# Kernel tuning notes

Measured on AMD Instinct MI355X. Metric: run time of the kernel, lower is better.

## Reference

```python
import jax, jax.numpy as jnp
import numpy as np

NUM_GROUPS = 8
EPS = 1e-6


def group_norm(x, gamma, beta):
    # x: [B, C, N] flattened spatial; GroupNorm over (channels-in-group, spatial)
    B, C, N = x.shape
    xg = x.reshape(B, NUM_GROUPS, C // NUM_GROUPS, N)
    mean = xg.mean(axis=(2, 3), keepdims=True)
    var = xg.var(axis=(2, 3), keepdims=True)
    xn = ((xg - mean) * jax.lax.rsqrt(var + EPS)).reshape(B, C, N)
    return xn * gamma[None, :, None] + beta[None, :, None]


def setup_inputs() -> dict:
    key = jax.random.key(0)
    ks = jax.random.split(key, 3)
    B, C, H, W, D = 4, 128, 16, 16, 16
    x = jax.random.normal(ks[0], (B, C, H, W, D), dtype=jnp.float32)
    gamma = jnp.ones((C,), dtype=jnp.float32)
    beta = jnp.zeros((C,), dtype=jnp.float32)
    init_scale = 0.1
    # default_init(scale): variance-scaling ~ scale/fan_avg uniform; approximate with scaled normal
    w_qkv = jax.random.normal(ks[1], (3 * C, C), dtype=jnp.float32) * np.sqrt(init_scale / C)
    b_qkv = jnp.zeros((3 * C,), dtype=jnp.float32)
    w_proj = jax.random.normal(ks[2], (C, C), dtype=jnp.float32) * np.sqrt(init_scale / C)
    b_proj = jnp.zeros((C,), dtype=jnp.float32)
    return {"x": x, "gamma": gamma, "beta": beta, "w_qkv": w_qkv,
            "b_qkv": b_qkv, "w_proj": w_proj, "b_proj": b_proj}


def reference(x, gamma, beta, w_qkv, b_qkv, w_proj, b_proj):
    B, C, H, W, D = x.shape
    N = H * W * D
    xf = x.reshape(B, C, N)
    xn = group_norm(xf, gamma, beta)
    # 1x1 Conv3d == channel GEMM: [3C, C] @ [B, C, N]
    qkv = jnp.einsum('oc,bcn->bon', w_qkv, xn) + b_qkv[None, :, None]
    q, k, v = jnp.split(qkv, 3, axis=1)  # each [B, C, N]
    scale = float(C) ** (-0.5)
    w = jnp.einsum('bcq,bck->bqk', q, k) * scale  # [B, N, N]
    w = jax.nn.softmax(w, axis=-1)
    h = jnp.einsum('bqk,bck->bcq', w, v)  # [B, C, N]
    h = jnp.einsum('oc,bcn->bon', w_proj, h) + b_proj[None, :, None]
    out = xf + h  # skip_scale = 1.0 (skip_scale=False)
    return out.reshape(B, C, H, W, D)
```

## Files before the change

### kernel.cpp

```cpp
#include <hip/hip_runtime.h>

typedef __bf16 bf16_t;
typedef bf16_t bf16x8 __attribute__((ext_vector_type(8)));
typedef float f32x4 __attribute__((ext_vector_type(4)));
typedef float f32x16 __attribute__((ext_vector_type(16)));
typedef unsigned short u16;
typedef unsigned int u32;

__device__ __forceinline__ float bfu2f(u32 h) {
  union { u32 u; float f; } v; v.u = h << 16;
  return v.f;
}
__device__ __forceinline__ void gll16(const void* g, void* l) {
  __builtin_amdgcn_global_load_lds((const __attribute__((address_space(1))) unsigned int*)g,
                                   (__attribute__((address_space(3))) unsigned int*)l, 16, 0, 0);
}
__device__ __forceinline__ u32 cvtpk(float lo, float hi) {
  u32 r;
  asm("v_cvt_pk_bf16_f32 %0, %1, %2" : "=v"(r) : "v"(lo), "v"(hi));
  return r;
}

__global__ __launch_bounds__(256) void gn_stats(const float* __restrict__ x,
                                                float* __restrict__ partial) {
  int bg = blockIdx.x >> 4, ck = blockIdx.x & 15;
  int tid = threadIdx.x;
  const float4* base = reinterpret_cast<const float4*>(x + (size_t)bg * 65536 + ck * 4096);
  float s = 0.f, sq = 0.f;
  #pragma unroll
  for (int j = 0; j < 4; ++j) {
    float4 v = base[j * 256 + tid];
    s += v.x + v.y + v.z + v.w;
    sq += v.x * v.x + v.y * v.y + v.z * v.z + v.w * v.w;
  }
  #pragma unroll
  for (int off = 32; off > 0; off >>= 1) {
    s += __shfl_down(s, off);
    sq += __shfl_down(sq, off);
  }
  __shared__ float red[8];
  int wid = tid >> 6;
  if ((tid & 63) == 0) { red[wid] = s; red[4 + wid] = sq; }
  __syncthreads();
  if (tid == 0) {
    float ts = red[0] + red[1] + red[2] + red[3];
    float tq = red[4] + red[5] + red[6] + red[7];
    partial[(bg * 16 + ck) * 2] = ts;
    partial[(bg * 16 + ck) * 2 + 1] = tq;
  }
}

__global__ __launch_bounds__(256) void gn_norm(const float* __restrict__ x,
                                               const float* __restrict__ gamma,
                                               const float* __restrict__ beta,
                                               const float* __restrict__ partial,
                                               u16* __restrict__ xnt) {
  int b = blockIdx.x >> 6, nc = blockIdx.x & 63;
  int tid = threadIdx.x;
  int cbase = (tid & 15) * 8;
  int g = cbase >> 4;
  float s = 0.f, sq = 0.f;
  #pragma unroll
  for (int k = 0; k < 16; ++k) {
    s += partial[((b * 8 + g) * 16 + k) * 2];
    sq += partial[((b * 8 + g) * 16 + k) * 2 + 1];
  }
  float mean = s * (1.f / 65536.f);
  float var = sq * (1.f / 65536.f) - mean * mean;
  float rstd = rsqrtf(var + 1e-6f);
  float ga[8], be[8];
  #pragma unroll
  for (int j = 0; j < 8; ++j) {
    ga[j] = gamma[cbase + j] * rstd;
    be[j] = beta[cbase + j] - mean * ga[j];
  }
  int n0 = nc * 64;
  #pragma unroll
  for (int it = 0; it < 4; ++it) {
    int n = n0 + it * 16 + (tid >> 4);
    union { u16 s[8]; uint4 u; } pk;
    #pragma unroll
    for (int j = 0; j < 8; ++j) {
      float v = x[((size_t)(b * 128 + cbase + j)) * 4096 + n] * ga[j] + be[j];
      pk.s[j] = __builtin_bit_cast(u16, (bf16_t)v);
    }
    *reinterpret_cast<uint4*>(xnt + ((size_t)(b * 4096 + n)) * 128 + cbase) = pk.u;
  }
}

__global__ __launch_bounds__(256) void qkv_kernel(const float* __restrict__ wq,
                                                  const float* __restrict__ bq,
                                                  const u16* __restrict__ xnt,
                                                  u16* __restrict__ qt,
                                                  u16* __restrict__ kt,
                                                  u16* __restrict__ vv) {
  __shared__ char aS[16384];
  __shared__ char bS[16384];
  int b = blockIdx.z;
  int o0 = blockIdx.y * 64;
  int n0 = blockIdx.x * 64;
  int tid = threadIdx.x;
  #pragma unroll
  for (int i = 0; i < 8; ++i) {
    int chunk = tid + (i << 8);
    int o = chunk >> 5, cj = (chunk & 31) << 2;
    float4 f = *reinterpret_cast<const float4*>(wq + (o0 + o) * 128 + cj);
    u16 h0 = __builtin_bit_cast(u16, (bf16_t)f.x);
    u16 h1 = __builtin_bit_cast(u16, (bf16_t)f.y);
    u16 h2 = __builtin_bit_cast(u16, (bf16_t)f.z);
    u16 h3 = __builtin_bit_cast(u16, (bf16_t)f.w);
    *reinterpret_cast<ushort4*>(aS + ((o * 256 + cj * 2) ^ ((o & 7) << 4))) = make_ushort4(h0, h1, h2, h3);
  }
  #pragma unroll
  for (int i = 0; i < 4; ++i) {
    int chunk = tid + (i << 8);
    int n = chunk >> 4, ch = chunk & 15;
    uint4 d = *reinterpret_cast<const uint4*>(xnt + ((size_t)(b * 4096 + n0 + n)) * 128 + ch * 8);
    *reinterpret_cast<uint4*>(bS + ((n * 256 + ch * 16) ^ ((n & 7) << 4))) = d;
  }
  __syncthreads();
  int w = tid >> 6, l = tid & 63, lr = l & 15, lg = l >> 4;
  f32x4 acc[4] = {{0,0,0,0},{0,0,0,0},{0,0,0,0},{0,0,0,0}};
  int orow = 16 * w + lr;
  #pragma unroll
  for (int kc = 0; kc < 4; ++kc) {
    int c2 = (lg * 8 + 32 * kc) * 2;
    bf16x8 a = *reinterpret_cast<const bf16x8*>(aS + ((orow * 256 + c2) ^ ((orow & 7) << 4)));
    #pragma unroll
    for (int fn = 0; fn < 4; ++fn) {
      int n = lr + 16 * fn;
      bf16x8 bb = *reinterpret_cast<const bf16x8*>(bS + ((n * 256 + c2) ^ ((n & 7) << 4)));
      acc[fn] = __builtin_amdgcn_mfma_f32_16x16x32_bf16(a, bb, acc[fn], 0, 0, 0);
    }
  }
  const float alpha = 0.12753325f;
  if (o0 < 256) {
    bool isq = (o0 < 128);
    __syncthreads();
    u16* tS = (u16*)aS;
    #pragma unroll
    for (int fn = 0; fn < 4; ++fn) {
      #pragma unroll
      for (int j = 0; j < 4; ++j) {
        int o_loc = 16 * w + lg * 4 + j;
        int n_loc = lr + 16 * fn;
        float v = acc[fn][j] + bq[o0 + o_loc];
        if (isq) v *= alpha;
        tS[o_loc * 68 + n_loc] = __builtin_bit_cast(u16, (bf16_t)v);
      }
    }
    __syncthreads();
    u16* dst = isq ? qt : kt;
    int obase = o0 & 127;
    #pragma unroll
    for (int it = 0; it < 2; ++it) {
      int n_l = (tid >> 3) + it * 32;
      int oc = (tid & 7) * 8;
      union { u16 s[8]; uint4 u; } pk;
      #pragma unroll
      for (int k2 = 0; k2 < 8; ++k2) pk.s[k2] = tS[(oc + k2) * 68 + n_l];
      *reinterpret_cast<uint4*>(dst + ((size_t)(b * 4096 + n0 + n_l)) * 128 + obase + oc) = pk.u;
    }
  } else {
    #pragma unroll
    for (int fn = 0; fn < 4; ++fn) {
      #pragma unroll
      for (int j = 0; j < 4; ++j) {
        int o_loc = 16 * w + lg * 4 + j;
        int n = n0 + lr + 16 * fn;
        float v = acc[fn][j] + bq[o0 + o_loc];
        ((bf16_t*)vv)[((size_t)(b * 128 + (o0 - 256) + o_loc)) * 4096 + n] = (bf16_t)v;
      }
    }
  }
}

__global__ __launch_bounds__(256, 2) void attn_kernel(const u16* __restrict__ qt,
                                                      const u16* __restrict__ kt,
                                                      const u16* __restrict__ vv,
                                                      u16* __restrict__ opart,
                                                      float* __restrict__ ml) {
  __shared__ char kS[2][16384];
  __shared__ char vS[2][16384];
  int b = blockIdx.z;
  int sp = blockIdx.y;
  int q0 = blockIdx.x * 128;
  int tid = threadIdx.x;
  int w = tid >> 6, l = tid & 63, lq = l & 31, h = l >> 5;

  bf16x8 qf[8];
  {
    const u16* qrow = qt + ((size_t)(b * 4096 + q0 + w * 32 + lq)) * 128 + h * 8;
    #pragma unroll
    for (int cs = 0; cs < 8; ++cs)
      qf[cs] = *reinterpret_cast<const bf16x8*>(qrow + cs * 16);
  }
  f32x16 acc[4];
  #pragma unroll
  for (int cc = 0; cc < 4; ++cc)
    #pragma unroll
    for (int i = 0; i < 16; ++i) acc[cc][i] = 0.f;
  float m2 = -1e30f, lsum = 0.f;

  const u16* ktb = kt + ((size_t)(b * 4096 + sp * 1024)) * 128;
  const u16* vvb = vv + ((size_t)b * 128) * 4096 + sp * 1024;

  auto stage = [&](int bufi, int kti) {
    #pragma unroll
    for (int i = 0; i < 4; ++i) {
      int n = (tid >> 4) + i * 16;
      int ck = (tid & 15) ^ (n & 7);
      gll16(ktb + (size_t)(kti * 64 + n) * 128 + ck * 8, kS[bufi] + tid * 16 + i * 4096);
    }
    #pragma unroll
    for (int i = 0; i < 4; ++i) {
      int c = (tid >> 3) + i * 32;
      int ck = (tid & 7) ^ (c & 7);
      gll16(vvb + (size_t)c * 4096 + kti * 64 + ck * 8, vS[bufi] + tid * 16 + i * 4096);
    }
  };

  stage(0, 0);
  __syncthreads();
  int buf = 0;

  for (int kti = 0; kti < 16; ++kti) {
    if (kti < 15) stage(buf ^ 1, kti + 1);

    f32x16 st0, st1;
    #pragma unroll
    for (int i = 0; i < 16; ++i) { st0[i] = 0.f; st1[i] = 0.f; }
    __builtin_amdgcn_s_setprio(1);
    #pragma unroll
    for (int cs = 0; cs < 8; ++cs) {
      int co = cs * 32 + h * 16;
      bf16x8 kf0 = *reinterpret_cast<const bf16x8*>(kS[buf] + ((lq * 256 + co) ^ ((lq & 7) << 4)));
      st0 = __builtin_amdgcn_mfma_f32_32x32x16_bf16(kf0, qf[cs], st0, 0, 0, 0);
      int kr1 = 32 + lq;
      bf16x8 kf1 = *reinterpret_cast<const bf16x8*>(kS[buf] + ((kr1 * 256 + co) ^ ((kr1 & 7) << 4)));
      st1 = __builtin_amdgcn_mfma_f32_32x32x16_bf16(kf1, qf[cs], st1, 0, 0, 0);
    }
    __builtin_amdgcn_s_setprio(0);

    float mt = st0[0];
    #pragma unroll
    for (int i = 1; i < 16; ++i) mt = fmaxf(mt, st0[i]);
    #pragma unroll
    for (int i = 0; i < 16; ++i) mt = fmaxf(mt, st1[i]);
    mt = fmaxf(mt, __shfl_xor(mt, 32));
    if (__any(mt > m2 + 8.f)) {
      float mn = fmaxf(m2, mt);
      float r = exp2f(m2 - mn);
      m2 = mn;
      lsum *= r;
      #pragma unroll
      for (int reg = 0; reg < 16; ++reg) {
        int qrow = (reg & 3) + 8 * (reg >> 2) + 4 * h;
        float rq = __shfl(r, qrow);
        #pragma unroll
        for (int cc = 0; cc < 4; ++cc) acc[cc][reg] *= rq;
      }
    }
    bf16x8 pa[4];
    #pragma unroll
    for (int ks = 0; ks < 2; ++ks) {
      float p[16];
      #pragma unroll
      for (int i = 0; i < 16; ++i) {
        float sv = (ks == 0) ? st0[i] : st1[i];
        p[i] = exp2f(sv - m2);
        lsum += p[i];
      }
      #pragma unroll
      for (int kk = 0; kk < 2; ++kk) {
        int r0 = kk * 8, r1 = kk * 8 + 4;
        u32 a1 = cvtpk(p[r0 + 0], p[r0 + 1]);
        u32 a2 = cvtpk(p[r0 + 2], p[r0 + 3]);
        u32 b1 = cvtpk(p[r1 + 0], p[r1 + 1]);
        u32 b2 = cvtpk(p[r1 + 2], p[r1 + 3]);
        u32 sa1 = (u32)__shfl_xor((int)a1, 32);
        u32 sa2 = (u32)__shfl_xor((int)a2, 32);
        u32 sb1 = (u32)__shfl_xor((int)b1, 32);
        u32 sb2 = (u32)__shfl_xor((int)b2, 32);
        union { u32 wd[4]; bf16x8 v; } af;
        af.wd[0] = h ? sb1 : a1;
        af.wd[1] = h ? sb2 : a2;
        af.wd[2] = h ? b1 : sa1;
        af.wd[3] = h ? b2 : sa2;
        pa[ks * 2 + kk] = af.v;
      }
    }
    __builtin_amdgcn_s_setprio(1);
    #pragma unroll
    for (int ks2 = 0; ks2 < 4; ++ks2) {
      int ko = ks2 * 32 + h * 16;
      #pragma unroll
      for (int cc = 0; cc < 4; ++cc) {
        int c = cc * 32 + lq;
        bf16x8 vf = *reinterpret_cast<const bf16x8*>(vS[buf] + ((c * 128 + ko) ^ ((c & 7) << 4)));
        acc[cc] = __builtin_amdgcn_mfma_f32_32x32x16_bf16(pa[ks2], vf, acc[cc], 0, 0, 0);
      }
    }
    __builtin_amdgcn_s_setprio(0);
    __syncthreads();
    buf ^= 1;
  }
  lsum += __shfl_xor(lsum, 32);
  #pragma unroll
  for (int reg = 0; reg < 16; ++reg) {
    int qrow = (reg & 3) + 8 * (reg >> 2) + 4 * h;
    size_t row = (size_t)(sp * 16384 + b * 4096 + q0 + w * 32 + qrow);
    bf16_t* orow = (bf16_t*)opart + row * 128 + lq;
    #pragma unroll
    for (int cc = 0; cc < 4; ++cc)
      orow[cc * 32] = (bf16_t)acc[cc][reg];
  }
  if (l < 32) {
    size_t row = (size_t)(sp * 16384 + b * 4096 + q0 + w * 32 + l);
    ml[row * 2] = m2;
    ml[row * 2 + 1] = lsum;
  }
}

__global__ __launch_bounds__(256) void proj_kernel(const float* __restrict__ wp,
                                                   const float* __restrict__ bp,
                                                   const u16* __restrict__ opart,
                                                   const float* __restrict__ ml,
                                                   const float* __restrict__ x,
                                                   float* __restrict__ out) {
  __shared__ char aS[16384];
  __shared__ char bS[16384];
  int b = blockIdx.z;
  int o0 = blockIdx.y * 64;
  int n0 = blockIdx.x * 64;
  int tid = threadIdx.x;
  #pragma unroll
  for (int i = 0; i < 8; ++i) {
    int chunk = tid + (i << 8);
    int o = chunk >> 5, cj = (chunk & 31) << 2;
    float4 f = *reinterpret_cast<const float4*>(wp + (o0 + o) * 128 + cj);
    u16 h0 = __builtin_bit_cast(u16, (bf16_t)f.x);
    u16 h1 = __builtin_bit_cast(u16, (bf16_t)f.y);
    u16 h2 = __builtin_bit_cast(u16, (bf16_t)f.z);
    u16 h3 = __builtin_bit_cast(u16, (bf16_t)f.w);
    *reinterpret_cast<ushort4*>(aS + ((o * 256 + cj * 2) ^ ((o & 7) << 4))) = make_ushort4(h0, h1, h2, h3);
  }
  #pragma unroll
  for (int i = 0; i < 4; ++i) {
    int chunk = tid + (i << 8);
    int n = chunk >> 4, ch = chunk & 15;
    size_t bn = (size_t)(b * 4096 + n0 + n);
    float m[4], lv[4];
    #pragma unroll
    for (int s = 0; s < 4; ++s) {
      m[s] = ml[((size_t)(s * 16384) + bn) * 2];
      lv[s] = ml[((size_t)(s * 16384) + bn) * 2 + 1];
    }
    float M = fmaxf(fmaxf(m[0], m[1]), fmaxf(m[2], m[3]));
    float wgt[4], L = 0.f;
    #pragma unroll
    for (int s = 0; s < 4; ++s) {
      wgt[s] = exp2f(m[s] - M);
      L += wgt[s] * lv[s];
    }
    float inv = 1.f / L;
    float o[8] = {0.f, 0.f, 0.f, 0.f, 0.f, 0.f, 0.f, 0.f};
    #pragma unroll
    for (int s = 0; s < 4; ++s) {
      uint4 pr = *reinterpret_cast<const uint4*>(opart + ((size_t)(s * 16384) + bn) * 128 + ch * 8);
      o[0] += wgt[s] * bfu2f(pr.x & 0xffffu);
      o[1] += wgt[s] * bfu2f(pr.x >> 16);
      o[2] += wgt[s] * bfu2f(pr.y & 0xffffu);
      o[3] += wgt[s] * bfu2f(pr.y >> 16);
      o[4] += wgt[s] * bfu2f(pr.z & 0xffffu);
      o[5] += wgt[s] * bfu2f(pr.z >> 16);
      o[6] += wgt[s] * bfu2f(pr.w & 0xffffu);
      o[7] += wgt[s] * bfu2f(pr.w >> 16);
    }
    u16 hh[8];
    #pragma unroll
    for (int e = 0; e < 8; ++e) hh[e] = __builtin_bit_cast(u16, (bf16_t)(o[e] * inv));
    uint4 packed;
    packed.x = (u32)hh[0] | ((u32)hh[1] << 16);
    packed.y = (u32)hh[2] | ((u32)hh[3] << 16);
    packed.z = (u32)hh[4] | ((u32)hh[5] << 16);
    packed.w = (u32)hh[6] | ((u32)hh[7] << 16);
    *reinterpret_cast<uint4*>(bS + ((n * 256 + ch * 16) ^ ((n & 7) << 4))) = packed;
  }
  __syncthreads();
  int w = tid >> 6, l = tid & 63, lr = l & 15, lg = l >> 4;
  f32x4 acc[4] = {{0,0,0,0},{0,0,0,0},{0,0,0,0},{0,0,0,0}};
  int orow = 16 * w + lr;
  #pragma unroll
  for (int kc = 0; kc < 4; ++kc) {
    int c2 = (lg * 8 + 32 * kc) * 2;
    bf16x8 a = *reinterpret_cast<const bf16x8*>(aS + ((orow * 256 + c2) ^ ((orow & 7) << 4)));
    #pragma unroll
    for (int fn = 0; fn < 4; ++fn) {
      int n = lr + 16 * fn;
      bf16x8 bb = *reinterpret_cast<const bf16x8*>(bS + ((n * 256 + c2) ^ ((n & 7) << 4)));
      acc[fn] = __builtin_amdgcn_mfma_f32_16x16x32_bf16(a, bb, acc[fn], 0, 0, 0);
    }
  }
  #pragma unroll
  for (int fn = 0; fn < 4; ++fn) {
    #pragma unroll
    for (int j = 0; j < 4; ++j) {
      int o = o0 + 16 * w + lg * 4 + j;
      int n = n0 + lr + 16 * fn;
      size_t idx = ((size_t)(b * 128 + o)) * 4096 + n;
      out[idx] = acc[fn][j] + bp[o] + x[idx];
    }
  }
}

extern "C" void kernel_launch(void* const* d_in, const int* in_sizes, int n_in,
                              void* d_out, int out_size, void* d_ws, size_t ws_size,
                              hipStream_t stream) {
  const float* x      = (const float*)d_in[0];
  const float* gamma  = (const float*)d_in[1];
  const float* beta   = (const float*)d_in[2];
  const float* w_qkv  = (const float*)d_in[3];
  const float* b_qkv  = (const float*)d_in[4];
  const float* w_proj = (const float*)d_in[5];
  const float* b_proj = (const float*)d_in[6];
  float* out = (float*)d_out;

  char* ws = (char*)d_ws;
  u16* xnt   = (u16*)(ws);
  u16* qt    = (u16*)(ws + (4u << 20));
  u16* kt    = (u16*)(ws + (8u << 20));
  u16* vv    = (u16*)(ws + (12u << 20));
  u16* opart = (u16*)(ws + (16u << 20));
  float* ml    = (float*)(ws + (48u << 20));
  float* parts = (float*)(ws + (49u << 20));

  hipLaunchKernelGGL(gn_stats, dim3(512), dim3(256), 0, stream, x, parts);
  hipLaunchKernelGGL(gn_norm, dim3(256), dim3(256), 0, stream, x, gamma, beta, parts, xnt);
  hipLaunchKernelGGL(qkv_kernel, dim3(64, 6, 4), dim3(256), 0, stream, w_qkv, b_qkv, xnt, qt, kt, vv);
  hipLaunchKernelGGL(attn_kernel, dim3(32, 4, 4), dim3(256), 0, stream, qt, kt, vv, opart, ml);
  hipLaunchKernelGGL(proj_kernel, dim3(64, 2, 4), dim3(256), 0, stream, w_proj, b_proj, opart, ml, x, out);
}
```

Baseline: 142.4 us.

## Coalesce GroupNorm transpose via LDS and reuse xnt tile across QKV outputs

gn_norm now reads x rows with contiguous float4 loads per channel. It transposes through a padded shared-memory tile, then writes xnt rows with 16-byte vector stores, replacing the strided scalar global reads. qkv_kernel now loops over three 64-row output chunks per block, so the xnt tile is staged once per block instead of once per chunk, and the grid shrinks from 6 to 2 in y. The cost is fewer blocks (512 instead of 1536), which means less parallelism, plus extra barriers per loop iteration and a separate shared transpose buffer.

```diff
diff --git a/kernel.cpp b/kernel.cpp
--- a/kernel.cpp
+++ b/kernel.cpp
@@ -55,10 +55,13 @@
                                                const float* __restrict__ beta,
                                                const float* __restrict__ partial,
                                                u16* __restrict__ xnt) {
+  __shared__ alignas(16) u16 tS[64 * 136];
   int b = blockIdx.x >> 6, nc = blockIdx.x & 63;
+  int n0 = nc * 64;
   int tid = threadIdx.x;
-  int cbase = (tid & 15) * 8;
-  int g = cbase >> 4;
+  int c = tid >> 1;
+  int nh = (tid & 1) * 32;
+  int g = c >> 4;
   float s = 0.f, sq = 0.f;
   #pragma unroll
   for (int k = 0; k < 16; ++k) {
@@ -68,24 +71,24 @@
   float mean = s * (1.f / 65536.f);
   float var = sq * (1.f / 65536.f) - mean * mean;
   float rstd = rsqrtf(var + 1e-6f);
-  float ga[8], be[8];
-  #pragma unroll
-  for (int j = 0; j < 8; ++j) {
-    ga[j] = gamma[cbase + j] * rstd;
-    be[j] = beta[cbase + j] - mean * ga[j];
-  }
-  int n0 = nc * 64;
-  #pragma unroll
-  for (int it = 0; it < 4; ++it) {
-    int n = n0 + it * 16 + (tid >> 4);
-    union { u16 s[8]; uint4 u; } pk;
-    #pragma unroll
-    for (int j = 0; j < 8; ++j) {
-      float v = x[((size_t)(b * 128 + cbase + j)) * 4096 + n] * ga[j] + be[j];
-      pk.s[j] = __builtin_bit_cast(u16, (bf16_t)v);
-    }
-    *reinterpret_cast<uint4*>(xnt + ((size_t)(b * 4096 + n)) * 128 + cbase) = pk.u;
-  }
+  float ga = gamma[c] * rstd;
+  float be = beta[c] - mean * ga;
+  const float4* xr4 = reinterpret_cast<const float4*>(x + ((size_t)(b * 128 + c)) * 4096 + n0 + nh);
+  #pragma unroll
+  for (int i = 0; i < 8; ++i) {
+    float4 v = xr4[i];
+    int nb = nh + i * 4;
+    tS[(nb + 0) * 136 + c] = __builtin_bit_cast(u16, (bf16_t)(v.x * ga + be));
+    tS[(nb + 1) * 136 + c] = __builtin_bit_cast(u16, (bf16_t)(v.y * ga + be));
+    tS[(nb + 2) * 136 + c] = __builtin_bit_cast(u16, (bf16_t)(v.z * ga + be));
+    tS[(nb + 3) * 136 + c] = __builtin_bit_cast(u16, (bf16_t)(v.w * ga + be));
+  }
+  __syncthreads();
+  int n = tid >> 2, cq = (tid & 3) * 32;
+  const uint4* src = reinterpret_cast<const uint4*>(tS + n * 136 + cq);
+  uint4 a0 = src[0], a1 = src[1], a2 = src[2], a3 = src[3];
+  uint4* dst = reinterpret_cast<uint4*>(xnt + ((size_t)(b * 4096 + n0 + n)) * 128 + cq);
+  dst[0] = a0; dst[1] = a1; dst[2] = a2; dst[3] = a3;
 }
 
 __global__ __launch_bounds__(256) void qkv_kernel(const float* __restrict__ wq,
@@ -96,21 +99,10 @@
                                                   u16* __restrict__ vv) {
   __shared__ char aS[16384];
   __shared__ char bS[16384];
+  __shared__ alignas(16) u16 tS[64 * 68];
   int b = blockIdx.z;
-  int o0 = blockIdx.y * 64;
   int n0 = blockIdx.x * 64;
   int tid = threadIdx.x;
-  #pragma unroll
-  for (int i = 0; i < 8; ++i) {
-    int chunk = tid + (i << 8);
-    int o = chunk >> 5, cj = (chunk & 31) << 2;
-    float4 f = *reinterpret_cast<const float4*>(wq + (o0 + o) * 128 + cj);
-    u16 h0 = __builtin_bit_cast(u16, (bf16_t)f.x);
-    u16 h1 = __builtin_bit_cast(u16, (bf16_t)f.y);
-    u16 h2 = __builtin_bit_cast(u16, (bf16_t)f.z);
-    u16 h3 = __builtin_bit_cast(u16, (bf16_t)f.w);
-    *reinterpret_cast<ushort4*>(aS + ((o * 256 + cj * 2) ^ ((o & 7) << 4))) = make_ushort4(h0, h1, h2, h3);
-  }
   #pragma unroll
   for (int i = 0; i < 4; ++i) {
     int chunk = tid + (i << 8);
@@ -118,60 +110,73 @@
     uint4 d = *reinterpret_cast<const uint4*>(xnt + ((size_t)(b * 4096 + n0 + n)) * 128 + ch * 8);
     *reinterpret_cast<uint4*>(bS + ((n * 256 + ch * 16) ^ ((n & 7) << 4))) = d;
   }
-  __syncthreads();
   int w = tid >> 6, l = tid & 63, lr = l & 15, lg = l >> 4;
-  f32x4 acc[4] = {{0,0,0,0},{0,0,0,0},{0,0,0,0},{0,0,0,0}};
-  int orow = 16 * w + lr;
-  #pragma unroll
-  for (int kc = 0; kc < 4; ++kc) {
-    int c2 = (lg * 8 + 32 * kc) * 2;
-    bf16x8 a = *reinterpret_cast<const bf16x8*>(aS + ((orow * 256 + c2) ^ ((orow & 7) << 4)));
-    #pragma unroll
-    for (int fn = 0; fn < 4; ++fn) {
-      int n = lr + 16 * fn;
-      bf16x8 bb = *reinterpret_cast<const bf16x8*>(bS + ((n * 256 + c2) ^ ((n & 7) << 4)));
-      acc[fn] = __builtin_amdgcn_mfma_f32_16x16x32_bf16(a, bb, acc[fn], 0, 0, 0);
-    }
-  }
   const float alpha = 0.12753325f;
-  if (o0 < 256) {
-    bool isq = (o0 < 128);
+  for (int oi = 0; oi < 3; ++oi) {
+    int o0 = (blockIdx.y * 3 + oi) * 64;
+    #pragma unroll
+    for (int i = 0; i < 8; ++i) {
+      int chunk = tid + (i << 8);
+      int o = chunk >> 5, cj = (chunk & 31) << 2;
+      float4 f = *reinterpret_cast<const float4*>(wq + (o0 + o) * 128 + cj);
+      u16 h0 = __builtin_bit_cast(u16, (bf16_t)f.x);
+      u16 h1 = __builtin_bit_cast(u16, (bf16_t)f.y);
+      u16 h2 = __builtin_bit_cast(u16, (bf16_t)f.z);
+      u16 h3 = __builtin_bit_cast(u16, (bf16_t)f.w);
+      *reinterpret_cast<ushort4*>(aS + ((o * 256 + cj * 2) ^ ((o & 7) << 4))) = make_ushort4(h0, h1, h2, h3);
+    }
     __syncthreads();
-    u16* tS = (u16*)aS;
-    #pragma unroll
-    for (int fn = 0; fn < 4; ++fn) {
-      #pragma unroll
-      for (int j = 0; j < 4; ++j) {
-        int o_loc = 16 * w + lg * 4 + j;
-        int n_loc = lr + 16 * fn;
-        float v = acc[fn][j] + bq[o0 + o_loc];
-        if (isq) v *= alpha;
-        tS[o_loc * 68 + n_loc] = __builtin_bit_cast(u16, (bf16_t)v);
+    f32x4 acc[4] = {{0,0,0,0},{0,0,0,0},{0,0,0,0},{0,0,0,0}};
+    int orow = 16 * w + lr;
+    #pragma unroll
+    for (int kc = 0; kc < 4; ++kc) {
+      int c2 = (lg * 8 + 32 * kc) * 2;
+      bf16x8 a = *reinterpret_cast<const bf16x8*>(aS + ((orow * 256 + c2) ^ ((orow & 7) << 4)));
+      #pragma unroll
+      for (int fn = 0; fn < 4; ++fn) {
+        int n = lr + 16 * fn;
+        bf16x8 bb = *reinterpret_cast<const bf16x8*>(bS + ((n * 256 + c2) ^ ((n & 7) << 4)));
+        acc[fn] = __builtin_amdgcn_mfma_f32_16x16x32_bf16(a, bb, acc[fn], 0, 0, 0);
+      }
+    }
+    if (o0 < 256) {
+      bool isq = (o0 < 128);
+      #pragma unroll
+      for (int fn = 0; fn < 4; ++fn) {
+        #pragma unroll
+        for (int j = 0; j < 4; ++j) {
+          int o_loc = 16 * w + lg * 4 + j;
+          int n_loc = lr + 16 * fn;
+          float v = acc[fn][j] + bq[o0 + o_loc];
+          if (isq) v *= alpha;
+          tS[o_loc * 68 + n_loc] = __builtin_bit_cast(u16, (bf16_t)v);
+        }
+      }
+      __syncthreads();
+      u16* dst = isq ? qt : kt;
+      int obase = o0 & 127;
+      #pragma unroll
+      for (int it = 0; it < 2; ++it) {
+        int n_l = (tid >> 3) + it * 32;
+        int oc = (tid & 7) * 8;
+        union { u16 s[8]; uint4 u; } pk;
+        #pragma unroll
+        for (int k2 = 0; k2 < 8; ++k2) pk.s[k2] = tS[(oc + k2) * 68 + n_l];
+        *reinterpret_cast<uint4*>(dst + ((size_t)(b * 4096 + n0 + n_l)) * 128 + obase + oc) = pk.u;
+      }
+    } else {
+      #pragma unroll
+      for (int fn = 0; fn < 4; ++fn) {
+        #pragma unroll
+        for (int j = 0; j < 4; ++j) {
+          int o_loc = 16 * w + lg * 4 + j;
+          int n = n0 + lr + 16 * fn;
+          float v = acc[fn][j] + bq[o0 + o_loc];
+          ((bf16_t*)vv)[((size_t)(b * 128 + (o0 - 256) + o_loc)) * 4096 + n] = (bf16_t)v;
+        }
       }
     }
     __syncthreads();
-    u16* dst = isq ? qt : kt;
-    int obase = o0 & 127;
-    #pragma unroll
-    for (int it = 0; it < 2; ++it) {
-      int n_l = (tid >> 3) + it * 32;
-      int oc = (tid & 7) * 8;
-      union { u16 s[8]; uint4 u; } pk;
-      #pragma unroll
-      for (int k2 = 0; k2 < 8; ++k2) pk.s[k2] = tS[(oc + k2) * 68 + n_l];
-      *reinterpret_cast<uint4*>(dst + ((size_t)(b * 4096 + n0 + n_l)) * 128 + obase + oc) = pk.u;
-    }
-  } else {
-    #pragma unroll
-    for (int fn = 0; fn < 4; ++fn) {
-      #pragma unroll
-      for (int j = 0; j < 4; ++j) {
-        int o_loc = 16 * w + lg * 4 + j;
-        int n = n0 + lr + 16 * fn;
-        float v = acc[fn][j] + bq[o0 + o_loc];
-        ((bf16_t*)vv)[((size_t)(b * 128 + (o0 - 256) + o_loc)) * 4096 + n] = (bf16_t)v;
-      }
-    }
   }
 }
 
@@ -437,7 +442,7 @@
 
   hipLaunchKernelGGL(gn_stats, dim3(512), dim3(256), 0, stream, x, parts);
   hipLaunchKernelGGL(gn_norm, dim3(256), dim3(256), 0, stream, x, gamma, beta, parts, xnt);
-  hipLaunchKernelGGL(qkv_kernel, dim3(64, 6, 4), dim3(256), 0, stream, w_qkv, b_qkv, xnt, qt, kt, vv);
+  hipLaunchKernelGGL(qkv_kernel, dim3(64, 2, 4), dim3(256), 0, stream, w_qkv, b_qkv, xnt, qt, kt, vv);
   hipLaunchKernelGGL(attn_kernel, dim3(32, 4, 4), dim3(256), 0, stream, qt, kt, vv, opart, ml);
   hipLaunchKernelGGL(proj_kernel, dim3(64, 2, 4), dim3(256), 0, stream, w_proj, b_proj, opart, ml, x, out);
 }
```

Result: no change. 142.2 us (-0.1%).
